# Optimization experiments

Measured on AMD Instinct MI355X. Metric: run time of the kernel, lower is better.

The kernel has to match this reference:

```python
import jax, jax.numpy as jnp
import numpy as np

K_TABLE = 8388608   # number of stored key/value pairs (2**23)
N_QUERY = 4194304   # number of lookups (2**22)
KEY_SPACE = 2147483647
DEFAULT_VALUE = -1  # DenseHashTable default_value for missing keys


def setup_inputs() -> dict:
    key = jax.random.key(0)
    k1, k2, k3, k4 = jax.random.split(key, 4)
    # Hash table contents, represented as a sorted key array + aligned values.
    table_keys = jnp.sort(jax.random.randint(k1, (K_TABLE,), 1, KEY_SPACE, dtype=jnp.int64))
    table_values = jax.random.randint(k2, (K_TABLE,), 0, 1000000, dtype=jnp.int64)
    # Queries: half random ids (mostly misses), half sampled from the table (hits).
    q_rand = jax.random.randint(k3, (N_QUERY // 2,), 1, KEY_SPACE, dtype=jnp.int64)
    hit_idx = jax.random.randint(k4, (N_QUERY // 2,), 0, K_TABLE, dtype=jnp.int64)
    q_hit = table_keys[hit_idx]
    query = jnp.concatenate([q_rand, q_hit])
    return {"query": query, "table_keys": table_keys, "table_values": table_values}


def reference(query, table_keys, table_values):
    # DenseHashTable.lookup: for each query id return its stored value,
    # or default_value (-1) if the key is absent. Implemented as a sorted
    # binary-search gather (same math: exact-match key -> value map).
    idx = jnp.searchsorted(table_keys, query)                 # [N]
    idx_c = jnp.clip(idx, 0, table_keys.shape[0] - 1)
    hit = table_keys[idx_c] == query                          # [N] bool
    out = jnp.where(hit, table_values[idx_c], jnp.int64(DEFAULT_VALUE))
    return out
```

## Files before the change

### kernel.cpp

```cpp
#include <hip/hip_runtime.h>


constexpr int WCAP = 1024;
constexpr int NBLK = 1 << 15;

__device__ __forceinline__ int lower_bound_u(const int* __restrict__ keys,
                                             int lo, int hi, unsigned t) {
    while (lo < hi) {
        int m = (lo + hi) >> 1;
        if ((unsigned)keys[m] < t) lo = m + 1; else hi = m;
    }
    return lo;
}

__global__ void block_index_kernel(const int* __restrict__ keys, int K,
                                   int* __restrict__ bstart) {
    int i = blockIdx.x * blockDim.x + threadIdx.x;
    if (i > NBLK) return;
    bstart[i] = lower_bound_u(keys, 0, K, ((unsigned)i) << 16);
}

__global__ void __launch_bounds__(256) build_rank_kernel(
        const int* __restrict__ keys, const int* __restrict__ vals, int K,
        const int* __restrict__ bstart, int4* __restrict__ table) {
    __shared__ int s_keys[WCAP];
    __shared__ int s_vals[WCAP];
    __shared__ int s_first[256];
    __shared__ int s_flag[256];
    __shared__ int s_ent[256][4];

    const int tid = threadIdx.x;
    const int wlo = bstart[blockIdx.x];
    const int whi = bstart[blockIdx.x + 1];
    const int wn = whi - wlo;
    const unsigned base_b = (unsigned)blockIdx.x << 8;

    s_flag[tid] = 0;
    s_ent[tid][0] = 0; s_ent[tid][1] = 0; s_ent[tid][2] = 0; s_ent[tid][3] = 0;

    if (wn <= WCAP) {
        for (int j = tid; j < wn; j += 256) {
            s_keys[j] = keys[wlo + j];
            s_vals[j] = vals[wlo + j];
        }
        __syncthreads();

        for (int j = tid; j < wn; j += 256) {
            unsigned b = ((unsigned)s_keys[j]) >> 8;
            bool first = (j == 0) || ((((unsigned)s_keys[j - 1]) >> 8) != b);
            if (first) s_first[b & 255u] = j;
        }
        __syncthreads();

        for (int j = tid; j < wn; j += 256) {
            int k = s_keys[j];
            unsigned lb = (((unsigned)k) >> 8) & 255u;
            int rank = j - s_first[lb];
            int v = s_vals[j];
            if (rank < 4 && (unsigned)v <= 0xFFFFFu) {
                s_ent[lb][rank] = (1 << 28) | (v << 8) | (k & 0xFF);
            } else {
                s_flag[lb] = 1;
            }
        }
        __syncthreads();

        int4 e;
        if (s_flag[tid]) e = make_int4(2 << 28, wlo + s_first[tid], 0, 0);
        else             e = make_int4(s_ent[tid][0], s_ent[tid][1],
                                       s_ent[tid][2], s_ent[tid][3]);
        table[base_b + tid] = e;
    } else {
        __syncthreads();
        unsigned b = base_b + tid;
        unsigned tlo = b << 8;
        unsigned thi = tlo + 256u;
        int lo = lower_bound_u(keys, wlo, whi, tlo);
        int w[4] = {0, 0, 0, 0};
        bool ok = true;
        int cnt = 0;
        int j = lo;
        while (j < whi && (unsigned)keys[j] < thi) {
            if (cnt >= 4) { ok = false; break; }
            int v = vals[j];
            if ((unsigned)v > 0xFFFFFu) { ok = false; break; }
            w[cnt] = (1 << 28) | (v << 8) | (keys[j] & 0xFF);
            ++cnt; ++j;
        }
        table[b] = ok ? make_int4(w[0], w[1], w[2], w[3])
                      : make_int4(2 << 28, lo, 0, 0);
    }
}

__device__ __forceinline__ int resolve_packed(int q, int4 e,
                                              const int* __restrict__ keys,
                                              const int* __restrict__ vals,
                                              int K) {
    if ((((unsigned)e.x) >> 28) == 2u) {
        for (int j = e.y; j < K; ++j) {
            int k = keys[j];
            if ((unsigned)k >= (unsigned)q) return (k == q) ? vals[j] : -1;
        }
        return -1;
    }
    int ql = q & 0xFF;
    int w;
    w = e.x; if ((((unsigned)w) >> 28) == 1u && (w & 0xFF) == ql) return (w >> 8) & 0xFFFFF;
    w = e.y; if ((((unsigned)w) >> 28) == 1u && (w & 0xFF) == ql) return (w >> 8) & 0xFFFFF;
    w = e.z; if ((((unsigned)w) >> 28) == 1u && (w & 0xFF) == ql) return (w >> 8) & 0xFFFFF;
    w = e.w; if ((((unsigned)w) >> 28) == 1u && (w & 0xFF) == ql) return (w >> 8) & 0xFFFFF;
    return -1;
}

__global__ void lookup_packed_kernel(const int* __restrict__ query,
                                     const int* __restrict__ keys,
                                     const int* __restrict__ vals,
                                     const int4* __restrict__ table,
                                     int* __restrict__ out,
                                     int N, int K, unsigned Bmask) {
    int half = (N + 1) >> 1;
    int i = blockIdx.x * blockDim.x + threadIdx.x;
    if (i >= half) return;
    int i1 = i + half;
    bool has1 = (i1 < N);
    int q0 = query[i];
    int q1 = has1 ? query[i1] : q0;
    int4 e0 = table[(((unsigned)q0) >> 8) & Bmask];
    int4 e1 = table[(((unsigned)q1) >> 8) & Bmask];
    out[i] = resolve_packed(q0, e0, keys, vals, K);
    if (has1) out[i1] = resolve_packed(q1, e1, keys, vals, K);
}

__global__ void lookup_bsearch_kernel(const int* __restrict__ query,
                                      const int* __restrict__ keys,
                                      const int* __restrict__ vals,
                                      int* __restrict__ out,
                                      int N, int K) {
    int i = blockIdx.x * blockDim.x + threadIdx.x;
    if (i >= N) return;
    unsigned q = (unsigned)query[i];
    int lo = lower_bound_u(keys, 0, K, q);
    int r = -1;
    if (lo < K && (unsigned)keys[lo] == q) r = vals[lo];
    out[i] = r;
}

extern "C" void kernel_launch(void* const* d_in, const int* in_sizes, int n_in,
                              void* d_out, int out_size, void* d_ws, size_t ws_size,
                              hipStream_t stream) {
    const int* query = (const int*)d_in[0];
    const int* keys  = (const int*)d_in[1];
    const int* vals  = (const int*)d_in[2];
    int* out = (int*)d_out;
    const int N = in_sizes[0];
    const int K = in_sizes[1];
    const int tb = 256;

    const size_t TABLE_BYTES = (size_t)16 << 23;
    const size_t IDX_BYTES   = (size_t)(NBLK + 1) * 4;

    if (TABLE_BYTES <= ws_size) {
        const unsigned B = 1u << 23;
        int4* table = (int4*)d_ws;
        int* bstart = (TABLE_BYTES + IDX_BYTES <= ws_size)
                          ? (int*)((char*)d_ws + TABLE_BYTES)
                          : (int*)d_out;
        block_index_kernel<<<(NBLK + 1 + tb - 1) / tb, tb, 0, stream>>>(keys, K, bstart);
        build_rank_kernel<<<NBLK, tb, 0, stream>>>(keys, vals, K, bstart, table);
        int half = (N + 1) >> 1;
        lookup_packed_kernel<<<(half + tb - 1) / tb, tb, 0, stream>>>(
            query, keys, vals, table, out, N, K, B - 1);
    } else {
        lookup_bsearch_kernel<<<(N + tb - 1) / tb, tb, 0, stream>>>(query, keys,
                                                                    vals, out, N, K);
    }
}
```

Baseline: 136.0 us.

## Add 2MB presence bitmap filter before packed table probe in lookup

Builds a 2 MB bitmap with one bit per 128-key range, so lookup threads can skip the 16-byte packed-table fetch for queries whose range holds no key. About half the queries are random misses, so this is meant to cut random table traffic, since the small bitmap is more likely to stay in cache. Each lookup thread now handles four queries to raise memory-level parallelism. The cost is an extra build kernel that scans all keys and a dependent bitmap load before each table probe. The path needs more workspace and falls back to the old path otherwise.

```diff
diff --git a/kernel.cpp b/kernel.cpp
--- a/kernel.cpp
+++ b/kernel.cpp
@@ -1,8 +1,9 @@
 #include <hip/hip_runtime.h>
 
 
-constexpr int WCAP = 1024;
-constexpr int NBLK = 1 << 15;
+constexpr int WCAP     = 1024;
+constexpr int NBLK     = 1 << 15;
+constexpr int BM_WORDS = 1 << 19;
 
 __device__ __forceinline__ int lower_bound_u(const int* __restrict__ keys,
                                              int lo, int hi, unsigned t) {
@@ -18,6 +19,25 @@
     int i = blockIdx.x * blockDim.x + threadIdx.x;
     if (i > NBLK) return;
     bstart[i] = lower_bound_u(keys, 0, K, ((unsigned)i) << 16);
+}
+
+__global__ void bitmap_build_kernel(const int* __restrict__ keys, int K,
+                                    const int* __restrict__ bstart,
+                                    unsigned* __restrict__ bitmap) {
+    int w = blockIdx.x * blockDim.x + threadIdx.x;
+    if (w >= BM_WORDS) return;
+    int blk = w >> 4;
+    int lo = bstart[blk], hi = bstart[blk + 1];
+    unsigned t0 = ((unsigned)w) << 12;
+    unsigned t1 = t0 + 4096u;
+    lo = lower_bound_u(keys, lo, hi, t0);
+    unsigned word = 0;
+    for (int j = lo; j < hi; ++j) {
+        unsigned k = (unsigned)keys[j];
+        if (k >= t1) break;
+        word |= 1u << ((k >> 7) & 31u);
+    }
+    bitmap[w] = word;
 }
 
 __global__ void __launch_bounds__(256) build_rank_kernel(
@@ -44,14 +64,12 @@
             s_vals[j] = vals[wlo + j];
         }
         __syncthreads();
-
         for (int j = tid; j < wn; j += 256) {
             unsigned b = ((unsigned)s_keys[j]) >> 8;
             bool first = (j == 0) || ((((unsigned)s_keys[j - 1]) >> 8) != b);
             if (first) s_first[b & 255u] = j;
         }
         __syncthreads();
-
         for (int j = tid; j < wn; j += 256) {
             int k = s_keys[j];
             unsigned lb = (((unsigned)k) >> 8) & 255u;
@@ -64,7 +82,6 @@
             }
         }
         __syncthreads();
-
         int4 e;
         if (s_flag[tid]) e = make_int4(2 << 28, wlo + s_first[tid], 0, 0);
         else             e = make_int4(s_ent[tid][0], s_ent[tid][1],
@@ -112,6 +129,39 @@
     return -1;
 }
 
+__global__ void lookup_bm_kernel(const int* __restrict__ query,
+                                 const int* __restrict__ keys,
+                                 const int* __restrict__ vals,
+                                 const int4* __restrict__ table,
+                                 const unsigned* __restrict__ bitmap,
+                                 int* __restrict__ out,
+                                 int N, int K, unsigned Bmask) {
+    int quarter = (N + 3) >> 2;
+    int i = blockIdx.x * blockDim.x + threadIdx.x;
+    if (i >= quarter) return;
+    int idx[4] = {i, i + quarter, i + 2 * quarter, i + 3 * quarter};
+    int q[4];
+    unsigned wbits[4];
+#pragma unroll
+    for (int c = 0; c < 4; ++c) q[c] = (idx[c] < N) ? query[idx[c]] : 1;
+#pragma unroll
+    for (int c = 0; c < 4; ++c) wbits[c] = bitmap[((unsigned)q[c]) >> 12];
+    bool probe[4];
+    int4 e[4];
+#pragma unroll
+    for (int c = 0; c < 4; ++c) {
+        unsigned bi = ((unsigned)q[c]) >> 7;
+        probe[c] = (idx[c] < N) && (((wbits[c] >> (bi & 31u)) & 1u) != 0u);
+        e[c] = probe[c] ? table[(((unsigned)q[c]) >> 8) & Bmask]
+                        : make_int4(0, 0, 0, 0);
+    }
+#pragma unroll
+    for (int c = 0; c < 4; ++c) {
+        if (idx[c] < N)
+            out[idx[c]] = probe[c] ? resolve_packed(q[c], e[c], keys, vals, K) : -1;
+    }
+}
+
 __global__ void lookup_packed_kernel(const int* __restrict__ query,
                                      const int* __restrict__ keys,
                                      const int* __restrict__ vals,
@@ -157,12 +207,25 @@
     const int tb = 256;
 
     const size_t TABLE_BYTES = (size_t)16 << 23;
-    const size_t IDX_BYTES   = (size_t)(NBLK + 1) * 4;
-
-    if (TABLE_BYTES <= ws_size) {
+    const size_t IDX_BYTES   = (((size_t)(NBLK + 1) * 4) + 63) & ~(size_t)63;
+    const size_t BM_BYTES    = (size_t)BM_WORDS * 4;
+
+    if (TABLE_BYTES + IDX_BYTES + BM_BYTES <= ws_size) {
         const unsigned B = 1u << 23;
         int4* table = (int4*)d_ws;
-        int* bstart = (TABLE_BYTES + IDX_BYTES <= ws_size)
+        int* bstart = (int*)((char*)d_ws + TABLE_BYTES);
+        unsigned* bitmap = (unsigned*)((char*)d_ws + TABLE_BYTES + IDX_BYTES);
+        block_index_kernel<<<(NBLK + 1 + tb - 1) / tb, tb, 0, stream>>>(keys, K, bstart);
+        bitmap_build_kernel<<<(BM_WORDS + tb - 1) / tb, tb, 0, stream>>>(keys, K,
+                                                                         bstart, bitmap);
+        build_rank_kernel<<<NBLK, tb, 0, stream>>>(keys, vals, K, bstart, table);
+        int quarter = (N + 3) >> 2;
+        lookup_bm_kernel<<<(quarter + tb - 1) / tb, tb, 0, stream>>>(
+            query, keys, vals, table, bitmap, out, N, K, B - 1);
+    } else if (TABLE_BYTES <= ws_size) {
+        const unsigned B = 1u << 23;
+        int4* table = (int4*)d_ws;
+        int* bstart = (TABLE_BYTES + (size_t)(NBLK + 1) * 4 <= ws_size)
                           ? (int*)((char*)d_ws + TABLE_BYTES)
                           : (int*)d_out;
         block_index_kernel<<<(NBLK + 1 + tb - 1) / tb, tb, 0, stream>>>(keys, K, bstart);
```

Result: slower. 164.6 us (+21.1%).
